# Performance work log

Measured on AMD Instinct MI355X. Metric: run time of the kernel, lower is better.

The kernel has to match this reference:

```python
import jax, jax.numpy as jnp
import numpy as np

K_NN = 5
COS_EPS = 1e-8  # torch cosine_similarity eps


def setup_inputs() -> dict:
    key = jax.random.key(0)
    ks = jax.random.split(key, 10)
    N1, N2, D, E, H = 2000, 2000, 63, 64, 8
    return {
        "lm_X": jax.random.normal(ks[0], (N1, D), jnp.float32),
        "lm_Y": jax.random.normal(ks[1], (N1, 2), jnp.float32),
        "tg_X": jax.random.normal(ks[2], (N2, D), jnp.float32),
        "tg_Y": jax.random.normal(ks[3], (N2, 2), jnp.float32),
        "lm_delay": jax.random.uniform(ks[4], (N1,), jnp.float32),
        "tg_delay": jax.random.uniform(ks[5], (N2,), jnp.float32),
        # learned params: embedding Linear(input_dim=D+1 -> E) and per-head score weights
        "W_emb": jax.random.normal(ks[6], (E, D + 1), jnp.float32) / np.sqrt(D + 1),
        "b_emb": jnp.zeros((E,), jnp.float32),
        "w1": jax.random.normal(ks[7], (E, H), jnp.float32),
        "w2": jax.random.normal(ks[8], (E, H), jnp.float32),
    }


def _knn_adj(X, k):
    # binary row-wise k-nearest-neighbour adjacency, self excluded
    n = X.shape[0]
    sq = jnp.sum(X * X, axis=1)
    d2 = sq[:, None] + sq[None, :] - 2.0 * (X @ X.T)  # [n, n] squared distances
    d2 = jnp.where(jnp.eye(n, dtype=bool), jnp.inf, d2)  # exclude self
    _, idx = jax.lax.top_k(-d2, k)  # k smallest distances -> [n, k]
    rows = jnp.arange(n)[:, None]
    return jnp.zeros((n, n), X.dtype).at[rows, idx].set(1.0)


def reference(lm_X, lm_Y, tg_X, tg_Y, lm_delay, tg_delay, W_emb, b_emb, w1, w2):
    N1 = lm_X.shape[0]
    N2 = tg_X.shape[0]
    N = N1 + N2
    k = K_NN

    # ---- community-KNN adjacency over landmarks, label aggregation ----
    adj_lm = _knn_adj(lm_X, k)                      # [N1, N1] binary, k ones per row
    y_pred = (adj_lm @ lm_Y) * (1.0 / k)            # [N1, 2]

    # ---- teacher adjacency: (1 - I) with lm block = adj_lm, tg block = 0 ----
    adj_teacher = 1.0 - jnp.eye(N, dtype=lm_X.dtype)
    adj_teacher = adj_teacher.at[:N1, :N1].set(adj_lm)
    adj_teacher = adj_teacher.at[N1:, N1:].set(0.0)

    # ---- node features + embedding ----
    lm_feat = jnp.concatenate([lm_X, lm_delay[:, None]], axis=1)  # [N1, D+1]
    tg_feat = jnp.concatenate([tg_X, tg_delay[:, None]], axis=1)  # [N2, D+1]
    feats = jnp.concatenate([lm_feat, tg_feat], axis=0)           # [N, D+1]
    e = feats @ W_emb.T + b_emb                                    # [N, E]

    # ---- multi-head cosine-similarity edge probabilities (all heads at once) ----
    a = e[:, None, :] * w1.T[None, :, :]            # [N, H, E] : e * w1[:, h]
    b = e[:, None, :] * w2.T[None, :, :]            # [N, H, E] : e * w2[:, h]
    na = jnp.linalg.norm(a, axis=-1)                # [N, H]
    nb = jnp.linalg.norm(b, axis=-1)                # [N, H]
    dot = jnp.einsum("nhe,mhe->nmh", a, b)          # [N, N, H]
    sim = dot / jnp.maximum(na[:, None, :] * nb[None, :, :], COS_EPS)
    alpha = jax.nn.sigmoid(sim)                      # [N, N, H]
    adj = jnp.mean(alpha, axis=-1)                   # [N, N]

    return (y_pred, adj, adj_teacher)
```

## Files before the change

kernel.cpp:

```cpp
#include <hip/hip_runtime.h>
#include <math.h>

#define N1 2000
#define N2 2000
#define NT 4000
#define D  63
#define E  64
#define H  8
#define KNN 5
#define NPAD 4032
#define MPAD 4096
#define NCB 8

typedef short bf16x8 __attribute__((ext_vector_type(8)));
typedef float f32x4  __attribute__((ext_vector_type(4)));

__device__ __forceinline__ unsigned short f2bf(float x) {
    unsigned u = __float_as_uint(x);
    u = (u + 0x7fffu + ((u >> 16) & 1u)) >> 16;
    return (unsigned short)u;
}

__device__ __forceinline__ bool dless(float d1, int i1, float d2v, int i2) {
    return d1 < d2v || (d1 == d2v && i1 < i2);
}

__device__ __forceinline__ void ins5(float bd[KNN], int bi[KNN], float d, int j) {
    if (dless(d, j, bd[KNN - 1], bi[KNN - 1])) {
        bd[KNN - 1] = d; bi[KNN - 1] = j;
        #pragma unroll
        for (int s = KNN - 1; s > 0; --s) {
            if (dless(bd[s], bi[s], bd[s - 1], bi[s - 1])) {
                float td = bd[s]; bd[s] = bd[s - 1]; bd[s - 1] = td;
                int ti = bi[s]; bi[s] = bi[s - 1]; bi[s - 1] = ti;
            }
        }
    }
}

__global__ __launch_bounds__(256) void k_knn(const float* __restrict__ X,
                                             float* __restrict__ part_d,
                                             int* __restrict__ part_i) {
    __shared__ float Xi[64][68];
    __shared__ float Xj[64][68];
    __shared__ float sqi[64];
    __shared__ float sqj[64];
    int cb = blockIdx.x, rb = blockIdx.y;
    int i0 = rb * 64;
    int tid = threadIdx.x;

    for (int t = tid; t < 64 * 64; t += 256) {
        int r = t >> 6, c = t & 63;
        int gi = min(i0 + r, N1 - 1);
        Xi[r][c] = (c < D) ? X[gi * D + c] : 0.f;
    }
    __syncthreads();
    if (tid < 64) {
        float s = 0.f;
        #pragma unroll
        for (int q = 0; q < 16; ++q) {
            float4 v = *(const float4*)&Xi[tid][4 * q];
            s += v.x * v.x + v.y * v.y + v.z * v.z + v.w * v.w;
        }
        sqi[tid] = s;
    }

    int tx = tid & 15, ty = tid >> 4;
    float bd[4][KNN]; int bi[4][KNN];
    #pragma unroll
    for (int ii = 0; ii < 4; ++ii)
        #pragma unroll
        for (int s = 0; s < KNN; ++s) { bd[ii][s] = __builtin_inff(); bi[ii][s] = 0x7fffffff; }

    for (int js = 0; js < 4; ++js) {
        int j0 = cb * 256 + js * 64;
        if (j0 >= N1) break;
        __syncthreads();
        for (int t = tid; t < 64 * 64; t += 256) {
            int r = t >> 6, c = t & 63;
            int gj = min(j0 + r, N1 - 1);
            Xj[r][c] = (c < D) ? X[gj * D + c] : 0.f;
        }
        __syncthreads();
        if (tid < 64) {
            float s = 0.f;
            #pragma unroll
            for (int q = 0; q < 16; ++q) {
                float4 v = *(const float4*)&Xj[tid][4 * q];
                s += v.x * v.x + v.y * v.y + v.z * v.z + v.w * v.w;
            }
            sqj[tid] = s;
        }
        __syncthreads();

        float acc[4][4];
        #pragma unroll
        for (int a = 0; a < 4; ++a)
            #pragma unroll
            for (int b = 0; b < 4; ++b) acc[a][b] = 0.f;

        #pragma unroll 4
        for (int kk = 0; kk < 16; ++kk) {
            float4 av[4], bv[4];
            #pragma unroll
            for (int ii = 0; ii < 4; ++ii) av[ii] = *(const float4*)&Xi[ty + 16 * ii][4 * kk];
            #pragma unroll
            for (int jj = 0; jj < 4; ++jj) bv[jj] = *(const float4*)&Xj[tx + 16 * jj][4 * kk];
            #pragma unroll
            for (int ii = 0; ii < 4; ++ii)
                #pragma unroll
                for (int jj = 0; jj < 4; ++jj)
                    acc[ii][jj] += av[ii].x * bv[jj].x + av[ii].y * bv[jj].y +
                                   av[ii].z * bv[jj].z + av[ii].w * bv[jj].w;
        }

        #pragma unroll
        for (int ii = 0; ii < 4; ++ii) {
            int gi = i0 + ty + 16 * ii;
            float si = sqi[ty + 16 * ii];
            #pragma unroll
            for (int jj = 0; jj < 4; ++jj) {
                int gj = j0 + tx + 16 * jj;
                if (gj < N1 && gj != gi) {
                    float dv = si + sqj[tx + 16 * jj] - 2.f * acc[ii][jj];
                    ins5(bd[ii], bi[ii], dv, gj);
                }
            }
        }
    }

    #pragma unroll
    for (int ii = 0; ii < 4; ++ii) {
        float wd[KNN]; int wi[KNN];
        #pragma unroll
        for (int s = 0; s < KNN; ++s) {
            float d = bd[ii][0]; int ix = bi[ii][0];
            #pragma unroll
            for (int m = 1; m < 16; m <<= 1) {
                float od = __shfl_xor(d, m, 64);
                int   oi = __shfl_xor(ix, m, 64);
                if (dless(od, oi, d, ix)) { d = od; ix = oi; }
            }
            wd[s] = d; wi[s] = ix;
            if (d == bd[ii][0] && ix == bi[ii][0]) {
                #pragma unroll
                for (int q = 0; q < KNN - 1; ++q) { bd[ii][q] = bd[ii][q + 1]; bi[ii][q] = bi[ii][q + 1]; }
                bd[ii][KNN - 1] = __builtin_inff(); bi[ii][KNN - 1] = 0x7fffffff;
            }
        }
        if (tx == 0) {
            int row = i0 + ty + 16 * ii;
            if (row < N1) {
                #pragma unroll
                for (int s = 0; s < KNN; ++s) {
                    part_d[row * (NCB * KNN) + cb * KNN + s] = wd[s];
                    part_i[row * (NCB * KNN) + cb * KNN + s] = wi[s];
                }
            }
        }
    }
}

__global__ __launch_bounds__(256) void k_merge(const float* __restrict__ part_d,
                                               const int* __restrict__ part_i,
                                               const float* __restrict__ lmY,
                                               float* __restrict__ ypred,
                                               int* __restrict__ idx) {
    int wave = threadIdx.x >> 6, lane = threadIdx.x & 63;
    int row = blockIdx.x * 4 + wave;
    float d = __builtin_inff(); int ix = 0x7fffffff;
    if (lane < NCB * KNN) {
        d  = part_d[row * (NCB * KNN) + lane];
        ix = part_i[row * (NCB * KNN) + lane];
    }
    float rd[KNN]; int ri[KNN];
    #pragma unroll
    for (int s = 0; s < KNN; ++s) {
        float md = d; int mi = ix;
        #pragma unroll
        for (int m = 1; m < 64; m <<= 1) {
            float od = __shfl_xor(md, m, 64);
            int   oi = __shfl_xor(mi, m, 64);
            if (dless(od, oi, md, mi)) { md = od; mi = oi; }
        }
        rd[s] = md; ri[s] = mi;
        if (md == d && mi == ix) { d = __builtin_inff(); ix = 0x7fffffff; }
    }
    if (lane == 0) {
        float y0 = 0.f, y1 = 0.f;
        #pragma unroll
        for (int s = 0; s < KNN; ++s) {
            int j = ri[s];
            y0 += lmY[j * 2];
            y1 += lmY[j * 2 + 1];
            idx[row * KNN + s] = j;
        }
        ypred[row * 2]     = y0 * 0.2f;
        ypred[row * 2 + 1] = y1 * 0.2f;
    }
}

__global__ __launch_bounds__(256) void k_prep(const float* __restrict__ lmX,
                                              const float* __restrict__ tgX,
                                              const float* __restrict__ lmD,
                                              const float* __restrict__ tgD,
                                              const float* __restrict__ W,
                                              const float* __restrict__ bias,
                                              const float* __restrict__ w1,
                                              const float* __restrict__ w2,
                                              unsigned short* __restrict__ AL,
                                              unsigned short* __restrict__ Bbuf,
                                              float* __restrict__ sB) {
    __shared__ float f[4][E];
    __shared__ float Wl[E][68];
    int tid = threadIdx.x, lane = tid & 63, wave = tid >> 6;
    int n = blockIdx.x * 4 + wave;
    #pragma unroll
    for (int k = 0; k < 4; ++k) {
        int g = k * 256 + tid;
        float4 v = ((const float4*)W)[g];
        int r = g >> 4, c = (g & 15) * 4;
        *(float4*)&Wl[r][c] = v;
    }
    int t = lane;
    if (t < D)  f[wave][t] = (n < N1) ? lmX[n * D + t] : tgX[(n - N1) * D + t];
    if (t == D) f[wave][t] = (n < N1) ? lmD[n] : tgD[n - N1];
    __syncthreads();
    float s0 = 0.f, s1 = 0.f, s2 = 0.f, s3 = 0.f;
    #pragma unroll
    for (int k = 0; k < 16; ++k) {
        float4 wv = *(const float4*)&Wl[t][4 * k];
        float4 fv = *(const float4*)&f[wave][4 * k];
        s0 += fv.x * wv.x; s1 += fv.y * wv.y; s2 += fv.z * wv.z; s3 += fv.w * wv.w;
    }
    const float en = bias[t] + (s0 + s1) + (s2 + s3);
    Bbuf[n * E + t] = f2bf(en);

    int kc = t >> 5, kq = (t >> 3) & 3, j = t & 7;
    int alane = kq * 16 + (n & 15);
    int nb = n >> 4;
    #pragma unroll
    for (int h = 0; h < H; ++h) {
        float a = en * w1[t * H + h];
        float b = en * w2[t * H + h];
        float na2 = a * a, nb2 = b * b;
        #pragma unroll
        for (int m = 32; m >= 1; m >>= 1) {
            na2 += __shfl_xor(na2, m, 64);
            nb2 += __shfl_xor(nb2, m, 64);
        }
        float val = a * w2[t * H + h] * rsqrtf(na2);
        AL[(((nb * 8 + h) << 1) + kc) * 512 + alane * 8 + j] = f2bf(val);
        if (t == h) sB[n * H + h] = rsqrtf(nb2);
    }
}

__global__ __launch_bounds__(256) void k_adjm(const unsigned short* __restrict__ AL,
                                              const unsigned short* __restrict__ Bbuf,
                                              const float* __restrict__ sB,
                                              const int* __restrict__ idx,
                                              float* __restrict__ adj,
                                              float* __restrict__ adjT) {
    __shared__ unsigned short Bt[256][68];
    int tid = threadIdx.x;
    int m0 = blockIdx.x * 256, n0 = blockIdx.y * 64;

    #pragma unroll
    for (int it = 0; it < 8; ++it) {
        int g = it * 256 + tid;
        int row = g >> 3, c = g & 7;
        *(bf16x8*)&Bt[row][c * 8] = *(const bf16x8*)&Bbuf[(m0 + row) * E + c * 8];
    }

    int wave = tid >> 6, lane = tid & 63;
    int l15 = lane & 15, kq = lane >> 4;
    int nb = blockIdx.y * 4 + wave;

    bf16x8 afr[H][2];
    #pragma unroll
    for (int h = 0; h < H; ++h)
        #pragma unroll
        for (int kc = 0; kc < 2; ++kc)
            afr[h][kc] = *(const bf16x8*)&AL[(((nb * 8 + h) << 1) + kc) * 512 + lane * 8];

    __syncthreads();

    int nebase = n0 + wave * 16 + kq * 4;
    int tr = tid >> 2, tcq = tid & 3;

    #pragma unroll 2
    for (int mt = 0; mt < 16; ++mt) {
        {
            int row = n0 + tr, col = m0 + mt * 16 + tcq * 4;
            if (row < NT && col < NT) {
                float v = ((row < N1) != (col < N1)) ? 1.f : 0.f;
                float4 o = {v, v, v, v};
                *(float4*)&adjT[row * NT + col] = o;
            }
        }

        int mrow = mt * 16 + l15;
        int mcol = m0 + mrow;
        bf16x8 b0 = *(const bf16x8*)&Bt[mrow][kq * 8];
        bf16x8 b1 = *(const bf16x8*)&Bt[mrow][32 + kq * 8];

        float sbv[H];
        *(f32x4*)&sbv[0] = *(const f32x4*)&sB[mcol * H + 0];
        *(f32x4*)&sbv[4] = *(const f32x4*)&sB[mcol * H + 4];

        f32x4 acc[H];
        #pragma unroll
        for (int h = 0; h < H; ++h) {
            acc[h] = (f32x4){0.f, 0.f, 0.f, 0.f};
            acc[h] = __builtin_amdgcn_mfma_f32_16x16x32_bf16(afr[h][0], b0, acc[h], 0, 0, 0);
            acc[h] = __builtin_amdgcn_mfma_f32_16x16x32_bf16(afr[h][1], b1, acc[h], 0, 0, 0);
        }

        bool mok = (mcol < NT);
        #pragma unroll
        for (int reg = 0; reg < 4; ++reg) {
            int ne = nebase + reg;
            float sum = 0.f;
            #pragma unroll
            for (int h = 0; h < H; ++h) {
                float x = acc[h][reg] * sbv[h];
                float u = x * x;
                float p = fmaf(u, 1.8919e-3f, -2.0833333e-2f);
                p = fmaf(u, p, 0.25f);
                sum = fmaf(x, p, sum);
            }
            if (mok && ne < NT) adj[ne * NT + mcol] = fmaf(sum, 0.125f, 0.5f);
        }
    }

    __syncthreads();
    for (int p = tid; p < 64 * KNN; p += 256) {
        int r = p / KNN, s = p - r * KNN;
        int row = n0 + r;
        if (row < N1) {
            int jx = idx[row * KNN + s];
            if (jx >= m0 && jx < m0 + 256) adjT[row * NT + jx] = 1.f;
        }
    }
}

extern "C" void kernel_launch(void* const* d_in, const int* in_sizes, int n_in,
                              void* d_out, int out_size, void* d_ws, size_t ws_size,
                              hipStream_t stream) {
    const float* lmX  = (const float*)d_in[0];
    const float* lmY  = (const float*)d_in[1];
    const float* tgX  = (const float*)d_in[2];
    const float* lmD  = (const float*)d_in[4];
    const float* tgD  = (const float*)d_in[5];
    const float* Wemb = (const float*)d_in[6];
    const float* bemb = (const float*)d_in[7];
    const float* w1   = (const float*)d_in[8];
    const float* w2   = (const float*)d_in[9];

    float* out   = (float*)d_out;
    float* ypred = out;
    float* adj   = out + 4000;
    float* adjT  = out + 4000 + 16000000;

    char* ws = (char*)d_ws;
    unsigned short* AL    = (unsigned short*)ws;
    unsigned short* Bbuf  = (unsigned short*)(ws + 4128768);
    float*          sB    = (float*)(ws + 4128768 + 524288);
    float*          partd = (float*)(ws + 4784128);
    int*            parti = (int*)  (ws + 5104128);
    int*            idx   = (int*)  (ws + 5424128);

    dim3 gk(NCB, 32);
    k_knn<<<gk, 256, 0, stream>>>(lmX, partd, parti);
    k_merge<<<N1 / 4, 256, 0, stream>>>(partd, parti, lmY, ypred, idx);
    k_prep<<<NT / 4, 256, 0, stream>>>(lmX, tgX, lmD, tgD, Wemb, bemb, w1, w2,
                                       AL, Bbuf, sB);
    dim3 ga(MPAD / 256, NPAD / 64);
    k_adjm<<<ga, 256, 0, stream>>>(AL, Bbuf, sB, idx, adj, adjT);
}
```

Measured before the change: 239.4 us.

## Split KNN column range into more blocks and move teacher-adjacency stores after MFMA loop

After: 221.4 us. 7.5% less time.

```diff
diff --git a/kernel.cpp b/kernel.cpp
--- a/kernel.cpp
+++ b/kernel.cpp
@@ -10,7 +10,7 @@
 #define KNN 5
 #define NPAD 4032
 #define MPAD 4096
-#define NCB 8
+#define NWIN 32
 
 typedef short bf16x8 __attribute__((ext_vector_type(8)));
 typedef float f32x4  __attribute__((ext_vector_type(4)));
@@ -46,85 +46,65 @@
     __shared__ float sqi[64];
     __shared__ float sqj[64];
     int cb = blockIdx.x, rb = blockIdx.y;
-    int i0 = rb * 64;
+    int i0 = rb * 64, j0 = cb * 64;
     int tid = threadIdx.x;
 
     for (int t = tid; t < 64 * 64; t += 256) {
         int r = t >> 6, c = t & 63;
         int gi = min(i0 + r, N1 - 1);
+        int gj = min(j0 + r, N1 - 1);
         Xi[r][c] = (c < D) ? X[gi * D + c] : 0.f;
-    }
-    __syncthreads();
-    if (tid < 64) {
+        Xj[r][c] = (c < D) ? X[gj * D + c] : 0.f;
+    }
+    __syncthreads();
+    if (tid < 128) {
+        int r = tid & 63;
+        const float* src = (tid < 64) ? &Xi[r][0] : &Xj[r][0];
         float s = 0.f;
         #pragma unroll
         for (int q = 0; q < 16; ++q) {
-            float4 v = *(const float4*)&Xi[tid][4 * q];
+            float4 v = *(const float4*)&src[4 * q];
             s += v.x * v.x + v.y * v.y + v.z * v.z + v.w * v.w;
         }
-        sqi[tid] = s;
-    }
+        if (tid < 64) sqi[r] = s; else sqj[r] = s;
+    }
+    __syncthreads();
 
     int tx = tid & 15, ty = tid >> 4;
+    float acc[4][4];
+    #pragma unroll
+    for (int a = 0; a < 4; ++a)
+        #pragma unroll
+        for (int b = 0; b < 4; ++b) acc[a][b] = 0.f;
+
+    #pragma unroll 4
+    for (int kk = 0; kk < 16; ++kk) {
+        float4 av[4], bv[4];
+        #pragma unroll
+        for (int ii = 0; ii < 4; ++ii) av[ii] = *(const float4*)&Xi[ty + 16 * ii][4 * kk];
+        #pragma unroll
+        for (int jj = 0; jj < 4; ++jj) bv[jj] = *(const float4*)&Xj[tx + 16 * jj][4 * kk];
+        #pragma unroll
+        for (int ii = 0; ii < 4; ++ii)
+            #pragma unroll
+            for (int jj = 0; jj < 4; ++jj)
+                acc[ii][jj] += av[ii].x * bv[jj].x + av[ii].y * bv[jj].y +
+                               av[ii].z * bv[jj].z + av[ii].w * bv[jj].w;
+    }
+
     float bd[4][KNN]; int bi[4][KNN];
     #pragma unroll
-    for (int ii = 0; ii < 4; ++ii)
+    for (int ii = 0; ii < 4; ++ii) {
         #pragma unroll
         for (int s = 0; s < KNN; ++s) { bd[ii][s] = __builtin_inff(); bi[ii][s] = 0x7fffffff; }
-
-    for (int js = 0; js < 4; ++js) {
-        int j0 = cb * 256 + js * 64;
-        if (j0 >= N1) break;
-        __syncthreads();
-        for (int t = tid; t < 64 * 64; t += 256) {
-            int r = t >> 6, c = t & 63;
-            int gj = min(j0 + r, N1 - 1);
-            Xj[r][c] = (c < D) ? X[gj * D + c] : 0.f;
-        }
-        __syncthreads();
-        if (tid < 64) {
-            float s = 0.f;
-            #pragma unroll
-            for (int q = 0; q < 16; ++q) {
-                float4 v = *(const float4*)&Xj[tid][4 * q];
-                s += v.x * v.x + v.y * v.y + v.z * v.z + v.w * v.w;
-            }
-            sqj[tid] = s;
-        }
-        __syncthreads();
-
-        float acc[4][4];
-        #pragma unroll
-        for (int a = 0; a < 4; ++a)
-            #pragma unroll
-            for (int b = 0; b < 4; ++b) acc[a][b] = 0.f;
-
-        #pragma unroll 4
-        for (int kk = 0; kk < 16; ++kk) {
-            float4 av[4], bv[4];
-            #pragma unroll
-            for (int ii = 0; ii < 4; ++ii) av[ii] = *(const float4*)&Xi[ty + 16 * ii][4 * kk];
-            #pragma unroll
-            for (int jj = 0; jj < 4; ++jj) bv[jj] = *(const float4*)&Xj[tx + 16 * jj][4 * kk];
-            #pragma unroll
-            for (int ii = 0; ii < 4; ++ii)
-                #pragma unroll
-                for (int jj = 0; jj < 4; ++jj)
-                    acc[ii][jj] += av[ii].x * bv[jj].x + av[ii].y * bv[jj].y +
-                                   av[ii].z * bv[jj].z + av[ii].w * bv[jj].w;
-        }
-
-        #pragma unroll
-        for (int ii = 0; ii < 4; ++ii) {
-            int gi = i0 + ty + 16 * ii;
-            float si = sqi[ty + 16 * ii];
-            #pragma unroll
-            for (int jj = 0; jj < 4; ++jj) {
-                int gj = j0 + tx + 16 * jj;
-                if (gj < N1 && gj != gi) {
-                    float dv = si + sqj[tx + 16 * jj] - 2.f * acc[ii][jj];
-                    ins5(bd[ii], bi[ii], dv, gj);
-                }
+        int gi = i0 + ty + 16 * ii;
+        float si = sqi[ty + 16 * ii];
+        #pragma unroll
+        for (int jj = 0; jj < 4; ++jj) {
+            int gj = j0 + tx + 16 * jj;
+            if (gj < N1 && gj != gi) {
+                float dv = si + sqj[tx + 16 * jj] - 2.f * acc[ii][jj];
+                ins5(bd[ii], bi[ii], dv, gj);
             }
         }
     }
@@ -153,8 +133,8 @@
             if (row < N1) {
                 #pragma unroll
                 for (int s = 0; s < KNN; ++s) {
-                    part_d[row * (NCB * KNN) + cb * KNN + s] = wd[s];
-                    part_i[row * (NCB * KNN) + cb * KNN + s] = wi[s];
+                    part_d[row * (NWIN * KNN) + cb * KNN + s] = wd[s];
+                    part_i[row * (NWIN * KNN) + cb * KNN + s] = wi[s];
                 }
             }
         }
@@ -168,11 +148,25 @@
                                                int* __restrict__ idx) {
     int wave = threadIdx.x >> 6, lane = threadIdx.x & 63;
     int row = blockIdx.x * 4 + wave;
-    float d = __builtin_inff(); int ix = 0x7fffffff;
-    if (lane < NCB * KNN) {
-        d  = part_d[row * (NCB * KNN) + lane];
-        ix = part_i[row * (NCB * KNN) + lane];
-    }
+    float ld[3]; int li[3];
+    #pragma unroll
+    for (int q = 0; q < 3; ++q) {
+        int c = lane + 64 * q;
+        if (c < NWIN * KNN) {
+            ld[q] = part_d[row * (NWIN * KNN) + c];
+            li[q] = part_i[row * (NWIN * KNN) + c];
+        } else { ld[q] = __builtin_inff(); li[q] = 0x7fffffff; }
+    }
+    #pragma unroll
+    for (int a = 0; a < 2; ++a)
+        #pragma unroll
+        for (int q = 0; q < 2; ++q)
+            if (dless(ld[q + 1], li[q + 1], ld[q], li[q])) {
+                float td = ld[q]; ld[q] = ld[q + 1]; ld[q + 1] = td;
+                int ti = li[q]; li[q] = li[q + 1]; li[q + 1] = ti;
+            }
+
+    float d = ld[0]; int ix = li[0]; int p = 0;
     float rd[KNN]; int ri[KNN];
     #pragma unroll
     for (int s = 0; s < KNN; ++s) {
@@ -184,7 +178,11 @@
             if (dless(od, oi, md, mi)) { md = od; mi = oi; }
         }
         rd[s] = md; ri[s] = mi;
-        if (md == d && mi == ix) { d = __builtin_inff(); ix = 0x7fffffff; }
+        if (md == d && mi == ix) {
+            ++p;
+            d  = (p < 3) ? ld[p] : __builtin_inff();
+            ix = (p < 3) ? li[p] : 0x7fffffff;
+        }
     }
     if (lane == 0) {
         float y0 = 0.f, y1 = 0.f;
@@ -286,19 +284,9 @@
     __syncthreads();
 
     int nebase = n0 + wave * 16 + kq * 4;
-    int tr = tid >> 2, tcq = tid & 3;
 
     #pragma unroll 2
     for (int mt = 0; mt < 16; ++mt) {
-        {
-            int row = n0 + tr, col = m0 + mt * 16 + tcq * 4;
-            if (row < NT && col < NT) {
-                float v = ((row < N1) != (col < N1)) ? 1.f : 0.f;
-                float4 o = {v, v, v, v};
-                *(float4*)&adjT[row * NT + col] = o;
-            }
-        }
-
         int mrow = mt * 16 + l15;
         int mcol = m0 + mrow;
         bf16x8 b0 = *(const bf16x8*)&Bt[mrow][kq * 8];
@@ -333,6 +321,18 @@
         }
     }
 
+    #pragma unroll
+    for (int it = 0; it < 16; ++it) {
+        int g = it * 256 + tid;
+        int r = g >> 6;
+        int col = m0 + (g & 63) * 4;
+        int row = n0 + r;
+        if (row < NT && col < NT) {
+            float v = ((row < N1) != (col < N1)) ? 1.f : 0.f;
+            float4 o = {v, v, v, v};
+            *(float4*)&adjT[row * NT + col] = o;
+        }
+    }
     __syncthreads();
     for (int p = tid; p < 64 * KNN; p += 256) {
         int r = p / KNN, s = p - r * KNN;
@@ -367,10 +367,10 @@
     unsigned short* Bbuf  = (unsigned short*)(ws + 4128768);
     float*          sB    = (float*)(ws + 4128768 + 524288);
     float*          partd = (float*)(ws + 4784128);
-    int*            parti = (int*)  (ws + 5104128);
-    int*            idx   = (int*)  (ws + 5424128);
-
-    dim3 gk(NCB, 32);
+    int*            parti = (int*)  (ws + 6064128);
+    int*            idx   = (int*)  (ws + 7344128);
+
+    dim3 gk(NWIN, 32);
     k_knn<<<gk, 256, 0, stream>>>(lmX, partd, parti);
     k_merge<<<N1 / 4, 256, 0, stream>>>(partd, parti, lmY, ypred, idx);
     k_prep<<<NT / 4, 256, 0, stream>>>(lmX, tgX, lmD, tgD, Wemb, bemb, w1, w2,
```
